# Kernel optimization log

Hardware: AMD Instinct MI355X
Metric: run time of the kernel (lower is better)

## Reference

```python
import jax, jax.numpy as jnp
import numpy as np

T = 32          # n_node_types
EXTRA = 3       # input_dim = T + 3
D = 9           # perfect binary tree depth -> N = 2**D - 1 = 511 nodes/plan
N = 2 ** D - 1
EMB = 64
HID = 64
FC = 64
OUT = 8         # N_METRICS
NS = 5          # N_SAMPLES
P = 2560        # number of plans (P // NS = 512 groups)
B = 512


def setup_inputs() -> dict:
    key = jax.random.key(0)
    ks = jax.random.split(key, 8)

    def lin(k, o, i):
        return (jax.random.normal(k, (o, i), jnp.float32) / np.sqrt(i)).astype(jnp.float32)

    x0 = jax.random.normal(ks[0], (P, N, T + EXTRA), jnp.float32)
    x = jax.random.uniform(ks[1], (B, P // NS), jnp.float32)
    return {
        "x": x,
        "x0": x0,
        "W_emb": lin(ks[2], EMB, T), "b_emb": jnp.zeros((EMB,), jnp.float32),
        "W0": lin(ks[3], HID, EMB + EXTRA), "b0": jnp.zeros((HID,), jnp.float32),
        "W1": lin(ks[4], HID, EMB + EXTRA + 2 * HID), "b1": jnp.zeros((HID,), jnp.float32),
        "Wfc1": lin(ks[5], FC, HID), "bfc1": jnp.zeros((FC,), jnp.float32),
        "Wfc2": lin(ks[6], OUT, FC), "bfc2": jnp.zeros((OUT,), jnp.float32),
    }


def reference(x, x0, W_emb, b_emb, W0, b0, W1, b1, Wfc1, bfc1, Wfc2, bfc2):
    # --- enc_dnn: per-node embed + concat(extra, children hiddens) + Linear + ReLU ---
    # node_emb = emb(xi[:T]); node_input = [node_emb, xi[T:], h_children...]
    emb = jnp.einsum('pnt,et->pne', x0[..., :T], W_emb) + b_emb    # [P,N,EMB]
    feats = jnp.concatenate([emb, x0[..., T:]], axis=-1)           # [P,N,EMB+3]
    # heap layout: node i's children are 2i+1, 2i+2; level l occupies [2^l-1, 2^{l+1}-1)
    lo = 2 ** (D - 1) - 1
    h = jax.nn.relu(jnp.einsum('pnf,hf->pnh', feats[:, lo:], W0) + b0)  # leaves
    for l in range(D - 2, -1, -1):  # structural loop over tree levels (fixed, small)
        lo, n = 2 ** l - 1, 2 ** l
        f = feats[:, lo:lo + n]
        inp = jnp.concatenate([f, h[:, 0::2], h[:, 1::2]], axis=-1)  # [emb|extra|h_left|h_right]
        h = jax.nn.relu(jnp.einsum('pnf,hf->pnh', inp, W1) + b1)
    h0 = h[:, 0]                                                   # root hidden, [P,HID]
    # --- agg_weight ---
    mean_h = h0.reshape(-1, NS, HID).mean(axis=1)                  # [P/NS, HID]
    weighted = x @ mean_h                                          # [B, HID]
    hid = jax.nn.relu(weighted @ Wfc1.T + bfc1)
    return hid @ Wfc2.T + bfc2                                     # [B, OUT]
```

## Files before the change

### kernel.cpp

```cpp
#include <hip/hip_runtime.h>
#include <hip/hip_bf16.h>


typedef __attribute__((ext_vector_type(8))) short s8v;
typedef __attribute__((ext_vector_type(4))) float f4v;
typedef unsigned short u16;
typedef unsigned int   u32;

__device__ __forceinline__ u16 f2bf(float f) {
    return __builtin_bit_cast(u16, __float2bfloat16(f));
}
__device__ __forceinline__ f4v mfma16(s8v a, s8v b, f4v c) {
    return __builtin_amdgcn_mfma_f32_16x16x32_bf16(a, b, c, 0, 0, 0);
}
#define SWZ(r) ((((r) & 1) | (((r) >> 1) & 6)) << 3)

__device__ __forceinline__ u32 pk2(float a, float b) {
    return (u32)f2bf(fmaxf(a, 0.f)) | ((u32)f2bf(fmaxf(b, 0.f)) << 16);
}
__device__ __forceinline__ s8v pkfrag(f4v h0, f4v h1) {
    int4 d;
    d.x = (int)pk2(h0[0], h0[1]); d.y = (int)pk2(h0[2], h0[3]);
    d.z = (int)pk2(h1[0], h1[1]); d.w = (int)pk2(h1[2], h1[3]);
    return __builtin_bit_cast(s8v, d);
}
__device__ __forceinline__ s8v xB0(const float* __restrict__ xr, int lq) {
    float4 A = *(const float4*)(xr + lq * 8);
    float4 B = *(const float4*)(xr + lq * 8 + 4);
    s8v r;
    r[0]=(short)f2bf(A.x); r[1]=(short)f2bf(A.y); r[2]=(short)f2bf(A.z); r[3]=(short)f2bf(A.w);
    r[4]=(short)f2bf(B.x); r[5]=(short)f2bf(B.y); r[6]=(short)f2bf(B.z); r[7]=(short)f2bf(B.w);
    return r;
}
__device__ __forceinline__ s8v xB1(const float* __restrict__ xr, int lq) {
    s8v r = (s8v){0,0,0,0,0,0,0,0};
    if (lq == 0) {
        float4 T = *(const float4*)(xr + 31);
        r[0]=(short)f2bf(T.y); r[1]=(short)f2bf(T.z); r[2]=(short)f2bf(T.w);
    }
    return r;
}
__device__ __forceinline__ s8v wread(const u16* w, int stride, int row, int ks, int lq) {
    return *(const s8v*)(w + row * stride + ks * 32 + lq * 8);
}
__device__ __forceinline__ f4v bias4(const float* __restrict__ b) {
    float4 t = *(const float4*)b; return (f4v){t.x, t.y, t.z, t.w};
}
__device__ __forceinline__ int sigp(int rho, int s, int h) {
    return 32*s + 4*h + ((rho & 12) << 1) + (rho & 3);
}

__global__ void prep_kernel(const float* __restrict__ W_emb, const float* __restrict__ b_emb,
                            const float* __restrict__ W0, const float* __restrict__ b0,
                            const float* __restrict__ W1, const float* __restrict__ b1,
                            u16* __restrict__ wt1, u16* __restrict__ wt0,
                            float* __restrict__ b1p, float* __restrict__ b0p)
{
    int idx = blockIdx.x * 256 + threadIdx.x;
    if (idx < 64 * 192) {
        int h = idx / 192, k = idx % 192;
        float v;
        if (k < 32) { v = 0.f; for (int e = 0; e < 64; e++) v = fmaf(W1[h*195+e], W_emb[e*32+k], v); }
        else if (k < 35)  v = W1[h*195 + 64 + (k - 32)];
        else if (k < 64)  v = 0.f;
        else              v = W1[h*195 + 67 + (k - 64)];
        wt1[h*192 + k] = f2bf(v);
    } else if (idx < 64*192 + 64*64) {
        int j = idx - 64*192; int h = j >> 6, k = j & 63;
        float v;
        if (k < 32)      { v = 0.f; for (int e = 0; e < 64; e++) v = fmaf(W0[h*67+e], W_emb[e*32+k], v); }
        else if (k < 35)   v = W0[h*67 + 64 + (k - 32)];
        else               v = 0.f;
        wt0[h*64 + k] = f2bf(v);
    } else if (idx < 64*192 + 64*64 + 64) {
        int h = idx - (64*192 + 64*64);
        float v = b1[h];
        for (int e = 0; e < 64; e++) v = fmaf(W1[h*195+e], b_emb[e], v);
        b1p[h] = v;
    } else if (idx < 64*192 + 64*64 + 128) {
        int h = idx - (64*192 + 64*64 + 64);
        float v = b0[h];
        for (int e = 0; e < 64; e++) v = fmaf(W0[h*67+e], b_emb[e], v);
        b0p[h] = v;
    }
}

__global__ __launch_bounds__(512, 2) void tree_chain(
    const float* __restrict__ x0,
    const u16* __restrict__ wt1g, const u16* __restrict__ wt0g,
    const float* __restrict__ b1p, const float* __restrict__ b0p,
    u16* __restrict__ h4)
{
    __shared__ __align__(16) u16 wt1s[64 * 200];
    __shared__ __align__(16) u16 wt0s[64 * 40 + 64];
    __shared__ __align__(16) u16 buf6[2 * 64 * 64];

    const int tid = threadIdx.x;
    const int l   = tid & 63;
    const int w   = tid >> 6;
    const int lq  = l >> 4;
    const int rho = l & 15;
    const int tsel = w >> 2;
    const int c    = w & 3;
    const int tree = blockIdx.x * 2 + tsel;
    const float* xb = x0 + (size_t)tree * 511 * 35;

    {
        u32* d1 = (u32*)wt1s; const u32* s1 = (const u32*)wt1g;
        #pragma unroll
        for (int t = 0; t < 12; t++) {
            int i = t*512 + tid;
            int row = i / 96, kk = i - row*96;
            d1[row*100 + kk] = s1[row*96 + kk];
        }
        u32* d0 = (u32*)wt0s; const u32* s0 = (const u32*)wt0g;
        #pragma unroll
        for (int t = 0; t < 3; t++) {
            int i = t*512 + tid;
            if (i < 1280) { int row = i / 20, kk = i - row*20; d0[row*20 + kk] = s0[row*32 + kk]; }
        }
        if (tid < 32) ((u32*)(wt0s + 64*40))[tid] = 0;
    }
    __syncthreads();

    s8v TLf[4][2];
    {
        s8v WL[4][2]; f4v bL[4];
        #pragma unroll
        for (int i = 0; i < 4; i++) {
            int s = i >> 1, h = i & 1;
            int sg = sigp(rho, s, h);
            WL[i][0] = wread(wt0s, 40, sg, 0, lq);
            WL[i][1] = wread(wt0s, 40, sg, 1, lq);
            bL[i] = bias4(b0p + 32*s + 8*lq + 4*h);
        }
        #pragma unroll
        for (int q = 0; q < 4; q++) {
            const float* xr = xb + (size_t)(255 + 64*c + 4*rho + q) * 35;
            s8v xa = xB0(xr, lq), xt = xB1(xr, lq);
            f4v a0 = bL[0], a1 = bL[1], a2 = bL[2], a3 = bL[3];
            a0 = mfma16(WL[0][0], xa, a0); a0 = mfma16(WL[0][1], xt, a0);
            a1 = mfma16(WL[1][0], xa, a1); a1 = mfma16(WL[1][1], xt, a1);
            a2 = mfma16(WL[2][0], xa, a2); a2 = mfma16(WL[2][1], xt, a2);
            a3 = mfma16(WL[3][0], xa, a3); a3 = mfma16(WL[3][1], xt, a3);
            TLf[q][0] = pkfrag(a0, a1);
            TLf[q][1] = pkfrag(a2, a3);
        }
    }

    s8v T7E0, T7E1, T7O0, T7O1;
    {
        f4v aE[4], aO[4];
        #pragma unroll
        for (int i = 0; i < 4; i++) {
            f4v b = bias4(b1p + 32*(i>>1) + 8*lq + 4*(i&1));
            aE[i] = b; aO[i] = b;
        }
        {
            const float* xrE = xb + (size_t)(127 + 32*c + 2*rho) * 35;
            const float* xrO = xrE + 35;
            s8v xE0 = xB0(xrE, lq), xE1 = xB1(xrE, lq);
            s8v xO0 = xB0(xrO, lq), xO1 = xB1(xrO, lq);
            #pragma unroll
            for (int i = 0; i < 4; i++) {
                int sg = sigp(rho, i>>1, i&1);
                s8v w0 = wread(wt1s, 200, sg, 0, lq);
                s8v w1 = wread(wt1s, 200, sg, 1, lq);
                aE[i] = mfma16(w0, xE0, aE[i]); aE[i] = mfma16(w1, xE1, aE[i]);
                aO[i] = mfma16(w0, xO0, aO[i]); aO[i] = mfma16(w1, xO1, aO[i]);
            }
        }
        #pragma unroll
        for (int i = 0; i < 4; i++) {
            int sg = sigp(rho, i>>1, i&1);
            s8v w2 = wread(wt1s, 200, sg, 2, lq);
            s8v w3 = wread(wt1s, 200, sg, 3, lq);
            s8v w4 = wread(wt1s, 200, sg, 4, lq);
            s8v w5 = wread(wt1s, 200, sg, 5, lq);
            aE[i] = mfma16(w2, TLf[0][0], aE[i]); aE[i] = mfma16(w3, TLf[0][1], aE[i]);
            aE[i] = mfma16(w4, TLf[1][0], aE[i]); aE[i] = mfma16(w5, TLf[1][1], aE[i]);
            aO[i] = mfma16(w2, TLf[2][0], aO[i]); aO[i] = mfma16(w3, TLf[2][1], aO[i]);
            aO[i] = mfma16(w4, TLf[3][0], aO[i]); aO[i] = mfma16(w5, TLf[3][1], aO[i]);
        }
        T7E0 = pkfrag(aE[0], aE[1]); T7E1 = pkfrag(aE[2], aE[3]);
        T7O0 = pkfrag(aO[0], aO[1]); T7O1 = pkfrag(aO[2], aO[3]);
    }

    {
        const float* xr6 = xb + (size_t)(63 + 16*c + rho) * 35;
        s8v x60 = xB0(xr6, lq), x61 = xB1(xr6, lq);
        u16* b6 = buf6 + tsel * 4096;
        int r6 = 16*c + rho;
        #pragma unroll
        for (int cc = 0; cc < 4; cc++) {
            f4v a = bias4(b1p + 16*cc + 4*lq);
            int sg = 16*cc + rho;
            s8v w0 = wread(wt1s, 200, sg, 0, lq);
            s8v w1 = wread(wt1s, 200, sg, 1, lq);
            s8v w2 = wread(wt1s, 200, sg, 2, lq);
            s8v w3 = wread(wt1s, 200, sg, 3, lq);
            s8v w4 = wread(wt1s, 200, sg, 4, lq);
            s8v w5 = wread(wt1s, 200, sg, 5, lq);
            a = mfma16(w0, x60, a);  a = mfma16(w1, x61, a);
            a = mfma16(w2, T7E0, a); a = mfma16(w3, T7E1, a);
            a = mfma16(w4, T7O0, a); a = mfma16(w5, T7O1, a);
            uint2 d; d.x = pk2(a[0], a[1]); d.y = pk2(a[2], a[3]);
            int col = (16*cc + 4*lq) ^ SWZ(r6);
            *(uint2*)(b6 + (size_t)r6 * 64 + col) = d;
        }
    }
    __syncthreads();

    if (c == 0) {
        const u16* b6r = buf6 + tsel * 4096;
        s8v ch5[2][2][2];
        #pragma unroll
        for (int d5 = 0; d5 < 2; d5++)
        #pragma unroll
        for (int pr = 0; pr < 2; pr++) {
            int row = 4*rho + 2*d5 + pr;
            int sw = SWZ(row);
            ch5[d5][pr][0] = *(const s8v*)(b6r + (size_t)row*64 + ((     8*lq) ^ sw));
            ch5[d5][pr][1] = *(const s8v*)(b6r + (size_t)row*64 + ((32 + 8*lq) ^ sw));
        }
        const float* xr5E = xb + (size_t)(31 + 2*rho) * 35;
        const float* xr5O = xr5E + 35;
        s8v x5E0 = xB0(xr5E, lq), x5E1 = xB1(xr5E, lq);
        s8v x5O0 = xB0(xr5O, lq), x5O1 = xB1(xr5O, lq);
        f4v aE[4], aO[4];
        #pragma unroll
        for (int i = 0; i < 4; i++) {
            f4v b = bias4(b1p + 32*(i>>1) + 8*lq + 4*(i&1));
            aE[i] = b; aO[i] = b;
        }
        #pragma unroll
        for (int i = 0; i < 4; i++) {
            int sg = sigp(rho, i>>1, i&1);
            s8v w0 = wread(wt1s, 200, sg, 0, lq);
            s8v w1 = wread(wt1s, 200, sg, 1, lq);
            s8v w2 = wread(wt1s, 200, sg, 2, lq);
            s8v w3 = wread(wt1s, 200, sg, 3, lq);
            s8v w4 = wread(wt1s, 200, sg, 4, lq);
            s8v w5 = wread(wt1s, 200, sg, 5, lq);
            aE[i] = mfma16(w0, x5E0, aE[i]); aE[i] = mfma16(w1, x5E1, aE[i]);
            aE[i] = mfma16(w2, ch5[0][0][0], aE[i]); aE[i] = mfma16(w3, ch5[0][0][1], aE[i]);
            aE[i] = mfma16(w4, ch5[0][1][0], aE[i]); aE[i] = mfma16(w5, ch5[0][1][1], aE[i]);
            aO[i] = mfma16(w0, x5O0, aO[i]); aO[i] = mfma16(w1, x5O1, aO[i]);
            aO[i] = mfma16(w2, ch5[1][0][0], aO[i]); aO[i] = mfma16(w3, ch5[1][0][1], aO[i]);
            aO[i] = mfma16(w4, ch5[1][1][0], aO[i]); aO[i] = mfma16(w5, ch5[1][1][1], aO[i]);
        }
        s8v L5E0 = pkfrag(aE[0], aE[1]), L5E1 = pkfrag(aE[2], aE[3]);
        s8v L5O0 = pkfrag(aO[0], aO[1]), L5O1 = pkfrag(aO[2], aO[3]);

        const float* xr4 = xb + (size_t)(15 + rho) * 35;
        s8v x40 = xB0(xr4, lq), x41 = xB1(xr4, lq);
        #pragma unroll
        for (int cc = 0; cc < 4; cc++) {
            f4v a = bias4(b1p + 16*cc + 4*lq);
            int sg = 16*cc + rho;
            s8v w0 = wread(wt1s, 200, sg, 0, lq);
            s8v w1 = wread(wt1s, 200, sg, 1, lq);
            s8v w2 = wread(wt1s, 200, sg, 2, lq);
            s8v w3 = wread(wt1s, 200, sg, 3, lq);
            s8v w4 = wread(wt1s, 200, sg, 4, lq);
            s8v w5 = wread(wt1s, 200, sg, 5, lq);
            a = mfma16(w0, x40, a);  a = mfma16(w1, x41, a);
            a = mfma16(w2, L5E0, a); a = mfma16(w3, L5E1, a);
            a = mfma16(w4, L5O0, a); a = mfma16(w5, L5O1, a);
            size_t base = ((size_t)tree*16 + rho) * 64 + 16*cc + 4*lq;
            *(u32*)(h4 + base)     = pk2(a[0], a[1]);
            *(u32*)(h4 + base + 2) = pk2(a[2], a[3]);
        }
    }
}

struct XL { float4 A, B, T; };
__device__ __forceinline__ s8v mk0(const XL& v) {
    s8v r;
    r[0]=(short)f2bf(v.A.x); r[1]=(short)f2bf(v.A.y); r[2]=(short)f2bf(v.A.z); r[3]=(short)f2bf(v.A.w);
    r[4]=(short)f2bf(v.B.x); r[5]=(short)f2bf(v.B.y); r[6]=(short)f2bf(v.B.z); r[7]=(short)f2bf(v.B.w);
    return r;
}
__device__ __forceinline__ s8v mk1(const XL& v) {
    s8v r = {0,0,0,0,0,0,0,0};
    r[0]=(short)f2bf(v.T.y); r[1]=(short)f2bf(v.T.z); r[2]=(short)f2bf(v.T.w);
    return r;
}

__global__ __launch_bounds__(64) void k3_tail(
    const float* __restrict__ x0,
    const u16* __restrict__ wt1, const float* __restrict__ b1p,
    const u16* __restrict__ h4, float* __restrict__ h0)
{
    __shared__ __align__(16) u16 tb0[32 * 64];
    __shared__ __align__(16) u16 tb1[32 * 64];
    const int l  = threadIdx.x;
    const int lq = l >> 4, lm = l & 15;
    const int p  = blockIdx.x;
    const float* xb = x0 + (size_t)p * 511 * 35;

    auto xload = [&](int lo) -> XL {
        const float* xr = xb + (size_t)(lo + lm) * 35;
        XL v;
        v.A = *(const float4*)(xr + lq * 8);
        v.B = *(const float4*)(xr + lq * 8 + 4);
        if (lq == 0) v.T = *(const float4*)(xr + 31);
        else         v.T = float4{0.f, 0.f, 0.f, 0.f};
        return v;
    };

    XL X3 = xload(7), X2 = xload(3), X1 = xload(1), X0v = xload(0);
    s8v ch[4];
    #pragma unroll
    for (int ks = 0; ks < 4; ks++) {
        int k0 = ks*32 + lq*8;
        int rr = 2*lm + (k0 >> 6);
        ch[ks] = *(const s8v*)(h4 + ((size_t)p*16 + rr)*64 + (k0 & 63));
    }

    s8v wB[6][4]; f4v bi[4];
    #pragma unroll
    for (int ct = 0; ct < 4; ct++) {
        int col = ct*16 + lm;
        #pragma unroll
        for (int ks = 0; ks < 6; ks++) wB[ks][ct] = *(const s8v*)(wt1 + col*192 + ks*32 + lq*8);
        float bv = b1p[col];
        bi[ct] = (f4v){bv, bv, bv, bv};
    }

    f4v acc[4];
    auto store_lds = [&](u16* buf) {
        #pragma unroll
        for (int r = 0; r < 4; r++) {
            int ro = lq*4 + r; int sw = SWZ(ro);
            #pragma unroll
            for (int ct = 0; ct < 4; ct++)
                buf[ro*64 + ((ct*16 + lm) ^ sw)] = f2bf(fmaxf(acc[ct][r], 0.f));
        }
        asm volatile("s_waitcnt lgkmcnt(0)" ::: "memory");
    };

    {
        s8v a0 = mk0(X3), a1 = mk1(X3);
        #pragma unroll
        for (int ct = 0; ct < 4; ct++) {
            acc[ct] = bi[ct];
            acc[ct] = mfma16(a0, wB[0][ct], acc[ct]);
            acc[ct] = mfma16(a1, wB[1][ct], acc[ct]);
        }
        #pragma unroll
        for (int ks = 0; ks < 4; ks++)
            #pragma unroll
            for (int ct = 0; ct < 4; ct++) acc[ct] = mfma16(ch[ks], wB[2 + ks][ct], acc[ct]);
        store_lds(tb0);
    }

    auto level = [&](const XL& xv, const u16* bufR) {
        s8v a0 = mk0(xv), a1 = mk1(xv);
        #pragma unroll
        for (int ct = 0; ct < 4; ct++) {
            acc[ct] = bi[ct];
            acc[ct] = mfma16(a0, wB[0][ct], acc[ct]);
            acc[ct] = mfma16(a1, wB[1][ct], acc[ct]);
        }
        #pragma unroll
        for (int ks = 0; ks < 4; ks++) {
            int k0 = ks*32 + lq*8;
            int rr = 2*lm + (k0 >> 6);
            s8v a = *(const s8v*)(bufR + rr*64 + ((k0 & 63) ^ SWZ(rr)));
            #pragma unroll
            for (int ct = 0; ct < 4; ct++) acc[ct] = mfma16(a, wB[2 + ks][ct], acc[ct]);
        }
    };
    level(X2, tb0); store_lds(tb1);
    level(X1, tb1); store_lds(tb0);
    level(X0v, tb0);
    if (lq == 0) {
        #pragma unroll
        for (int ct = 0; ct < 4; ct++)
            h0[(size_t)p*64 + ct*16 + lm] = fmaxf(acc[ct][0], 0.f);
    }
}

__global__ void mean_kernel(const float* __restrict__ h0, float* __restrict__ mh)
{
    int idx = blockIdx.x * blockDim.x + threadIdx.x;
    if (idx < 512 * 64) {
        int g = idx >> 6, h = idx & 63;
        float s = 0.f;
        #pragma unroll
        for (int q = 0; q < 5; q++) s += h0[(size_t)(g * 5 + q) * 64 + h];
        mh[idx] = s * 0.2f;
    }
}

__global__ __launch_bounds__(64) void head_kernel(const float* __restrict__ x,
                                                  const float* __restrict__ mh,
                                                  const float* __restrict__ Wfc1,
                                                  const float* __restrict__ bfc1,
                                                  const float* __restrict__ Wfc2,
                                                  const float* __restrict__ bfc2,
                                                  float* __restrict__ out)
{
    __shared__ float sw[64];
    __shared__ float sh[64];
    int b = blockIdx.x, h = threadIdx.x;

    float a0 = 0.f, a1 = 0.f, a2 = 0.f, a3 = 0.f;
    const float* xr = x + (size_t)b * 512;
    for (int g = 0; g < 512; g += 4) {
        a0 = fmaf(xr[g + 0], mh[(g + 0) * 64 + h], a0);
        a1 = fmaf(xr[g + 1], mh[(g + 1) * 64 + h], a1);
        a2 = fmaf(xr[g + 2], mh[(g + 2) * 64 + h], a2);
        a3 = fmaf(xr[g + 3], mh[(g + 3) * 64 + h], a3);
    }
    sw[h] = (a0 + a1) + (a2 + a3);
    __syncthreads();

    float acc = bfc1[h];
    #pragma unroll 8
    for (int k = 0; k < 64; k++) acc = fmaf(Wfc1[h * 64 + k], sw[k], acc);
    sh[h] = fmaxf(acc, 0.f);
    __syncthreads();

    if (h < 8) {
        float o = bfc2[h];
        #pragma unroll 8
        for (int f = 0; f < 64; f++) o = fmaf(Wfc2[h * 64 + f], sh[f], o);
        out[(size_t)b * 8 + h] = o;
    }
}

extern "C" void kernel_launch(void* const* d_in, const int* in_sizes, int n_in,
                              void* d_out, int out_size, void* d_ws, size_t ws_size,
                              hipStream_t stream)
{
    (void)in_sizes; (void)n_in; (void)out_size; (void)ws_size;
    const float* x     = (const float*)d_in[0];
    const float* x0    = (const float*)d_in[1];
    const float* W_emb = (const float*)d_in[2];
    const float* b_emb = (const float*)d_in[3];
    const float* W0    = (const float*)d_in[4];
    const float* b0    = (const float*)d_in[5];
    const float* W1    = (const float*)d_in[6];
    const float* b1    = (const float*)d_in[7];
    const float* Wfc1  = (const float*)d_in[8];
    const float* bfc1  = (const float*)d_in[9];
    const float* Wfc2  = (const float*)d_in[10];
    const float* bfc2  = (const float*)d_in[11];
    float* out = (float*)d_out;

    u16* wt1   = (u16*)d_ws;
    u16* wt0   = wt1 + 64 * 192;
    float* b1p = (float*)(wt0 + 64 * 64);
    float* b0p = b1p + 64;
    u16* h4    = (u16*)(b0p + 64);
    float* h0  = (float*)(h4 + (size_t)2560 * 16 * 64);
    float* mh  = h0 + 2560 * 64;

    prep_kernel<<<65, 256, 0, stream>>>(W_emb, b_emb, W0, b0, W1, b1, wt1, wt0, b1p, b0p);
    tree_chain<<<1280, 512, 0, stream>>>(x0, wt1, wt0, b1p, b0p, h4);
    k3_tail<<<2560, 64, 0, stream>>>(x0, wt1, b1p, h4, h0);
    mean_kernel<<<128, 256, 0, stream>>>(h0, mh);
    head_kernel<<<512, 64, 0, stream>>>(x, mh, Wfc1, bfc1, Wfc2, bfc2, out);
}
```

Before: 95.69 us.

## Fuse tree tail into chain kernel and process four trees per block

Merges the separate tail kernel (levels 3..0) into the main tree kernel, so the level-4 hiddens stay in LDS instead of round-tripping through a global h4 buffer, and one launch is removed. Each block now handles four trees, with each wave pair processing two trees through the leaf-to-level-6 stages. The weight load into LDS is amortised over twice as many trees. Levels 5 and below now run on only 4 of 8 waves, one tree per wave, which leaves half the block idle in the tail. LDS use also grows, which may lower occupancy.

Measured after the change: 88.57 us, median of 2. 7.4% less time.

```diff
diff --git a/kernel.cpp b/kernel.cpp
--- a/kernel.cpp
+++ b/kernel.cpp
@@ -85,25 +85,27 @@
     }
 }
 
-__global__ __launch_bounds__(512, 2) void tree_chain(
+__global__ __launch_bounds__(512, 2) void tree_all(
     const float* __restrict__ x0,
     const u16* __restrict__ wt1g, const u16* __restrict__ wt0g,
     const float* __restrict__ b1p, const float* __restrict__ b0p,
-    u16* __restrict__ h4)
+    float* __restrict__ h0out)
 {
     __shared__ __align__(16) u16 wt1s[64 * 200];
     __shared__ __align__(16) u16 wt0s[64 * 40 + 64];
-    __shared__ __align__(16) u16 buf6[2 * 64 * 64];
+    __shared__ __align__(16) u16 buf6[4 * 64 * 64];
 
     const int tid = threadIdx.x;
     const int l   = tid & 63;
     const int w   = tid >> 6;
     const int lq  = l >> 4;
     const int rho = l & 15;
-    const int tsel = w >> 2;
+    const int pair = w >> 2;
     const int c    = w & 3;
-    const int tree = blockIdx.x * 2 + tsel;
-    const float* xb = x0 + (size_t)tree * 511 * 35;
+    const int tA = blockIdx.x * 4 + 2 * pair;
+    const int tB = tA + 1;
+    const float* xbA = x0 + (size_t)tA * 511 * 35;
+    const float* xbB = x0 + (size_t)tB * 511 * 35;
 
     {
         u32* d1 = (u32*)wt1s; const u32* s1 = (const u32*)wt1g;
@@ -123,77 +125,96 @@
     }
     __syncthreads();
 
-    s8v TLf[4][2];
+    s8v TLA[4][2], TLB[4][2];
     {
         s8v WL[4][2]; f4v bL[4];
         #pragma unroll
         for (int i = 0; i < 4; i++) {
-            int s = i >> 1, h = i & 1;
-            int sg = sigp(rho, s, h);
+            int sg = sigp(rho, i >> 1, i & 1);
             WL[i][0] = wread(wt0s, 40, sg, 0, lq);
             WL[i][1] = wread(wt0s, 40, sg, 1, lq);
-            bL[i] = bias4(b0p + 32*s + 8*lq + 4*h);
+            bL[i] = bias4(b0p + 32*(i>>1) + 8*lq + 4*(i&1));
         }
         #pragma unroll
         for (int q = 0; q < 4; q++) {
-            const float* xr = xb + (size_t)(255 + 64*c + 4*rho + q) * 35;
-            s8v xa = xB0(xr, lq), xt = xB1(xr, lq);
-            f4v a0 = bL[0], a1 = bL[1], a2 = bL[2], a3 = bL[3];
-            a0 = mfma16(WL[0][0], xa, a0); a0 = mfma16(WL[0][1], xt, a0);
-            a1 = mfma16(WL[1][0], xa, a1); a1 = mfma16(WL[1][1], xt, a1);
-            a2 = mfma16(WL[2][0], xa, a2); a2 = mfma16(WL[2][1], xt, a2);
-            a3 = mfma16(WL[3][0], xa, a3); a3 = mfma16(WL[3][1], xt, a3);
-            TLf[q][0] = pkfrag(a0, a1);
-            TLf[q][1] = pkfrag(a2, a3);
-        }
-    }
-
-    s8v T7E0, T7E1, T7O0, T7O1;
+            const float* xrA = xbA + (size_t)(255 + 64*c + 4*rho + q) * 35;
+            const float* xrB = xbB + (size_t)(255 + 64*c + 4*rho + q) * 35;
+            s8v xaA = xB0(xrA, lq), xtA = xB1(xrA, lq);
+            s8v xaB = xB0(xrB, lq), xtB = xB1(xrB, lq);
+            f4v aA[4], aB[4];
+            #pragma unroll
+            for (int i = 0; i < 4; i++) { aA[i] = bL[i]; aB[i] = bL[i]; }
+            #pragma unroll
+            for (int i = 0; i < 4; i++) {
+                aA[i] = mfma16(WL[i][0], xaA, aA[i]);
+                aA[i] = mfma16(WL[i][1], xtA, aA[i]);
+                aB[i] = mfma16(WL[i][0], xaB, aB[i]);
+                aB[i] = mfma16(WL[i][1], xtB, aB[i]);
+            }
+            TLA[q][0] = pkfrag(aA[0], aA[1]); TLA[q][1] = pkfrag(aA[2], aA[3]);
+            TLB[q][0] = pkfrag(aB[0], aB[1]); TLB[q][1] = pkfrag(aB[2], aB[3]);
+        }
+    }
+
+    s8v A7[4], B7[4];
     {
-        f4v aE[4], aO[4];
+        f4v aAE[4], aAO[4], aBE[4], aBO[4];
         #pragma unroll
         for (int i = 0; i < 4; i++) {
             f4v b = bias4(b1p + 32*(i>>1) + 8*lq + 4*(i&1));
-            aE[i] = b; aO[i] = b;
+            aAE[i] = b; aAO[i] = b; aBE[i] = b; aBO[i] = b;
         }
         {
-            const float* xrE = xb + (size_t)(127 + 32*c + 2*rho) * 35;
-            const float* xrO = xrE + 35;
-            s8v xE0 = xB0(xrE, lq), xE1 = xB1(xrE, lq);
-            s8v xO0 = xB0(xrO, lq), xO1 = xB1(xrO, lq);
+            const float* xrAE = xbA + (size_t)(127 + 32*c + 2*rho) * 35;
+            const float* xrBE = xbB + (size_t)(127 + 32*c + 2*rho) * 35;
+            s8v xAE0 = xB0(xrAE, lq),      xAE1 = xB1(xrAE, lq);
+            s8v xAO0 = xB0(xrAE + 35, lq), xAO1 = xB1(xrAE + 35, lq);
+            s8v xBE0 = xB0(xrBE, lq),      xBE1 = xB1(xrBE, lq);
+            s8v xBO0 = xB0(xrBE + 35, lq), xBO1 = xB1(xrBE + 35, lq);
             #pragma unroll
             for (int i = 0; i < 4; i++) {
-                int sg = sigp(rho, i>>1, i&1);
+                int sg = sigp(rho, i >> 1, i & 1);
                 s8v w0 = wread(wt1s, 200, sg, 0, lq);
                 s8v w1 = wread(wt1s, 200, sg, 1, lq);
-                aE[i] = mfma16(w0, xE0, aE[i]); aE[i] = mfma16(w1, xE1, aE[i]);
-                aO[i] = mfma16(w0, xO0, aO[i]); aO[i] = mfma16(w1, xO1, aO[i]);
+                aAE[i] = mfma16(w0, xAE0, aAE[i]); aAE[i] = mfma16(w1, xAE1, aAE[i]);
+                aAO[i] = mfma16(w0, xAO0, aAO[i]); aAO[i] = mfma16(w1, xAO1, aAO[i]);
+                aBE[i] = mfma16(w0, xBE0, aBE[i]); aBE[i] = mfma16(w1, xBE1, aBE[i]);
+                aBO[i] = mfma16(w0, xBO0, aBO[i]); aBO[i] = mfma16(w1, xBO1, aBO[i]);
             }
         }
         #pragma unroll
         for (int i = 0; i < 4; i++) {
-            int sg = sigp(rho, i>>1, i&1);
+            int sg = sigp(rho, i >> 1, i & 1);
             s8v w2 = wread(wt1s, 200, sg, 2, lq);
             s8v w3 = wread(wt1s, 200, sg, 3, lq);
             s8v w4 = wread(wt1s, 200, sg, 4, lq);
             s8v w5 = wread(wt1s, 200, sg, 5, lq);
-            aE[i] = mfma16(w2, TLf[0][0], aE[i]); aE[i] = mfma16(w3, TLf[0][1], aE[i]);
-            aE[i] = mfma16(w4, TLf[1][0], aE[i]); aE[i] = mfma16(w5, TLf[1][1], aE[i]);
-            aO[i] = mfma16(w2, TLf[2][0], aO[i]); aO[i] = mfma16(w3, TLf[2][1], aO[i]);
-            aO[i] = mfma16(w4, TLf[3][0], aO[i]); aO[i] = mfma16(w5, TLf[3][1], aO[i]);
-        }
-        T7E0 = pkfrag(aE[0], aE[1]); T7E1 = pkfrag(aE[2], aE[3]);
-        T7O0 = pkfrag(aO[0], aO[1]); T7O1 = pkfrag(aO[2], aO[3]);
+            aAE[i] = mfma16(w2, TLA[0][0], aAE[i]); aAE[i] = mfma16(w3, TLA[0][1], aAE[i]);
+            aAE[i] = mfma16(w4, TLA[1][0], aAE[i]); aAE[i] = mfma16(w5, TLA[1][1], aAE[i]);
+            aAO[i] = mfma16(w2, TLA[2][0], aAO[i]); aAO[i] = mfma16(w3, TLA[2][1], aAO[i]);
+            aAO[i] = mfma16(w4, TLA[3][0], aAO[i]); aAO[i] = mfma16(w5, TLA[3][1], aAO[i]);
+            aBE[i] = mfma16(w2, TLB[0][0], aBE[i]); aBE[i] = mfma16(w3, TLB[0][1], aBE[i]);
+            aBE[i] = mfma16(w4, TLB[1][0], aBE[i]); aBE[i] = mfma16(w5, TLB[1][1], aBE[i]);
+            aBO[i] = mfma16(w2, TLB[2][0], aBO[i]); aBO[i] = mfma16(w3, TLB[2][1], aBO[i]);
+            aBO[i] = mfma16(w4, TLB[3][0], aBO[i]); aBO[i] = mfma16(w5, TLB[3][1], aBO[i]);
+        }
+        A7[0] = pkfrag(aAE[0], aAE[1]); A7[1] = pkfrag(aAE[2], aAE[3]);
+        A7[2] = pkfrag(aAO[0], aAO[1]); A7[3] = pkfrag(aAO[2], aAO[3]);
+        B7[0] = pkfrag(aBE[0], aBE[1]); B7[1] = pkfrag(aBE[2], aBE[3]);
+        B7[2] = pkfrag(aBO[0], aBO[1]); B7[3] = pkfrag(aBO[2], aBO[3]);
     }
 
     {
-        const float* xr6 = xb + (size_t)(63 + 16*c + rho) * 35;
-        s8v x60 = xB0(xr6, lq), x61 = xB1(xr6, lq);
-        u16* b6 = buf6 + tsel * 4096;
+        const float* xrA6 = xbA + (size_t)(63 + 16*c + rho) * 35;
+        const float* xrB6 = xbB + (size_t)(63 + 16*c + rho) * 35;
+        s8v xA0 = xB0(xrA6, lq), xA1 = xB1(xrA6, lq);
+        s8v xBv0 = xB0(xrB6, lq), xBv1 = xB1(xrB6, lq);
+        u16* slA = buf6 + (2*pair) * 4096;
+        u16* slB = slA + 4096;
         int r6 = 16*c + rho;
+        int sw6 = SWZ(r6);
         #pragma unroll
         for (int cc = 0; cc < 4; cc++) {
-            f4v a = bias4(b1p + 16*cc + 4*lq);
             int sg = 16*cc + rho;
             s8v w0 = wread(wt1s, 200, sg, 0, lq);
             s8v w1 = wread(wt1s, 200, sg, 1, lq);
@@ -201,18 +222,28 @@
             s8v w3 = wread(wt1s, 200, sg, 3, lq);
             s8v w4 = wread(wt1s, 200, sg, 4, lq);
             s8v w5 = wread(wt1s, 200, sg, 5, lq);
-            a = mfma16(w0, x60, a);  a = mfma16(w1, x61, a);
-            a = mfma16(w2, T7E0, a); a = mfma16(w3, T7E1, a);
-            a = mfma16(w4, T7O0, a); a = mfma16(w5, T7O1, a);
-            uint2 d; d.x = pk2(a[0], a[1]); d.y = pk2(a[2], a[3]);
-            int col = (16*cc + 4*lq) ^ SWZ(r6);
-            *(uint2*)(b6 + (size_t)r6 * 64 + col) = d;
+            f4v bb = bias4(b1p + 16*cc + 4*lq);
+            f4v aA = bb, aB = bb;
+            aA = mfma16(w0, xA0, aA);  aA = mfma16(w1, xA1, aA);
+            aA = mfma16(w2, A7[0], aA); aA = mfma16(w3, A7[1], aA);
+            aA = mfma16(w4, A7[2], aA); aA = mfma16(w5, A7[3], aA);
+            aB = mfma16(w0, xBv0, aB); aB = mfma16(w1, xBv1, aB);
+            aB = mfma16(w2, B7[0], aB); aB = mfma16(w3, B7[1], aB);
+            aB = mfma16(w4, B7[2], aB); aB = mfma16(w5, B7[3], aB);
+            int col = (16*cc + 4*lq) ^ sw6;
+            uint2 dA; dA.x = pk2(aA[0], aA[1]); dA.y = pk2(aA[2], aA[3]);
+            uint2 dB; dB.x = pk2(aB[0], aB[1]); dB.y = pk2(aB[2], aB[3]);
+            *(uint2*)(slA + (size_t)r6 * 64 + col) = dA;
+            *(uint2*)(slB + (size_t)r6 * 64 + col) = dB;
         }
     }
     __syncthreads();
 
-    if (c == 0) {
-        const u16* b6r = buf6 + tsel * 4096;
+    if (w < 4) {
+        const int tree = blockIdx.x * 4 + w;
+        u16* slice = buf6 + w * 4096;
+        const float* xb = x0 + (size_t)tree * 511 * 35;
+
         s8v ch5[2][2][2];
         #pragma unroll
         for (int d5 = 0; d5 < 2; d5++)
@@ -220,13 +251,12 @@
         for (int pr = 0; pr < 2; pr++) {
             int row = 4*rho + 2*d5 + pr;
             int sw = SWZ(row);
-            ch5[d5][pr][0] = *(const s8v*)(b6r + (size_t)row*64 + ((     8*lq) ^ sw));
-            ch5[d5][pr][1] = *(const s8v*)(b6r + (size_t)row*64 + ((32 + 8*lq) ^ sw));
+            ch5[d5][pr][0] = *(const s8v*)(slice + (size_t)row*64 + ((     8*lq) ^ sw));
+            ch5[d5][pr][1] = *(const s8v*)(slice + (size_t)row*64 + ((32 + 8*lq) ^ sw));
         }
         const float* xr5E = xb + (size_t)(31 + 2*rho) * 35;
-        const float* xr5O = xr5E + 35;
-        s8v x5E0 = xB0(xr5E, lq), x5E1 = xB1(xr5E, lq);
-        s8v x5O0 = xB0(xr5O, lq), x5O1 = xB1(xr5O, lq);
+        s8v x5E0 = xB0(xr5E, lq),      x5E1 = xB1(xr5E, lq);
+        s8v x5O0 = xB0(xr5E + 35, lq), x5O1 = xB1(xr5E + 35, lq);
         f4v aE[4], aO[4];
         #pragma unroll
         for (int i = 0; i < 4; i++) {
@@ -235,7 +265,7 @@
         }
         #pragma unroll
         for (int i = 0; i < 4; i++) {
-            int sg = sigp(rho, i>>1, i&1);
+            int sg = sigp(rho, i >> 1, i & 1);
             s8v w0 = wread(wt1s, 200, sg, 0, lq);
             s8v w1 = wread(wt1s, 200, sg, 1, lq);
             s8v w2 = wread(wt1s, 200, sg, 2, lq);
@@ -252,133 +282,77 @@
         s8v L5E0 = pkfrag(aE[0], aE[1]), L5E1 = pkfrag(aE[2], aE[3]);
         s8v L5O0 = pkfrag(aO[0], aO[1]), L5O1 = pkfrag(aO[2], aO[3]);
 
-        const float* xr4 = xb + (size_t)(15 + rho) * 35;
-        s8v x40 = xB0(xr4, lq), x41 = xB1(xr4, lq);
-        #pragma unroll
-        for (int cc = 0; cc < 4; cc++) {
-            f4v a = bias4(b1p + 16*cc + 4*lq);
-            int sg = 16*cc + rho;
-            s8v w0 = wread(wt1s, 200, sg, 0, lq);
-            s8v w1 = wread(wt1s, 200, sg, 1, lq);
-            s8v w2 = wread(wt1s, 200, sg, 2, lq);
-            s8v w3 = wread(wt1s, 200, sg, 3, lq);
-            s8v w4 = wread(wt1s, 200, sg, 4, lq);
-            s8v w5 = wread(wt1s, 200, sg, 5, lq);
-            a = mfma16(w0, x40, a);  a = mfma16(w1, x41, a);
-            a = mfma16(w2, L5E0, a); a = mfma16(w3, L5E1, a);
-            a = mfma16(w4, L5O0, a); a = mfma16(w5, L5O1, a);
-            size_t base = ((size_t)tree*16 + rho) * 64 + 16*cc + 4*lq;
-            *(u32*)(h4 + base)     = pk2(a[0], a[1]);
-            *(u32*)(h4 + base + 2) = pk2(a[2], a[3]);
-        }
-    }
-}
-
-struct XL { float4 A, B, T; };
-__device__ __forceinline__ s8v mk0(const XL& v) {
-    s8v r;
-    r[0]=(short)f2bf(v.A.x); r[1]=(short)f2bf(v.A.y); r[2]=(short)f2bf(v.A.z); r[3]=(short)f2bf(v.A.w);
-    r[4]=(short)f2bf(v.B.x); r[5]=(short)f2bf(v.B.y); r[6]=(short)f2bf(v.B.z); r[7]=(short)f2bf(v.B.w);
-    return r;
-}
-__device__ __forceinline__ s8v mk1(const XL& v) {
-    s8v r = {0,0,0,0,0,0,0,0};
-    r[0]=(short)f2bf(v.T.y); r[1]=(short)f2bf(v.T.z); r[2]=(short)f2bf(v.T.w);
-    return r;
-}
-
-__global__ __launch_bounds__(64) void k3_tail(
-    const float* __restrict__ x0,
-    const u16* __restrict__ wt1, const float* __restrict__ b1p,
-    const u16* __restrict__ h4, float* __restrict__ h0)
-{
-    __shared__ __align__(16) u16 tb0[32 * 64];
-    __shared__ __align__(16) u16 tb1[32 * 64];
-    const int l  = threadIdx.x;
-    const int lq = l >> 4, lm = l & 15;
-    const int p  = blockIdx.x;
-    const float* xb = x0 + (size_t)p * 511 * 35;
-
-    auto xload = [&](int lo) -> XL {
-        const float* xr = xb + (size_t)(lo + lm) * 35;
-        XL v;
-        v.A = *(const float4*)(xr + lq * 8);
-        v.B = *(const float4*)(xr + lq * 8 + 4);
-        if (lq == 0) v.T = *(const float4*)(xr + 31);
-        else         v.T = float4{0.f, 0.f, 0.f, 0.f};
-        return v;
-    };
-
-    XL X3 = xload(7), X2 = xload(3), X1 = xload(1), X0v = xload(0);
-    s8v ch[4];
-    #pragma unroll
-    for (int ks = 0; ks < 4; ks++) {
-        int k0 = ks*32 + lq*8;
-        int rr = 2*lm + (k0 >> 6);
-        ch[ks] = *(const s8v*)(h4 + ((size_t)p*16 + rr)*64 + (k0 & 63));
-    }
-
-    s8v wB[6][4]; f4v bi[4];
-    #pragma unroll
-    for (int ct = 0; ct < 4; ct++) {
-        int col = ct*16 + lm;
-        #pragma unroll
-        for (int ks = 0; ks < 6; ks++) wB[ks][ct] = *(const s8v*)(wt1 + col*192 + ks*32 + lq*8);
-        float bv = b1p[col];
-        bi[ct] = (f4v){bv, bv, bv, bv};
-    }
-
-    f4v acc[4];
-    auto store_lds = [&](u16* buf) {
-        #pragma unroll
-        for (int r = 0; r < 4; r++) {
-            int ro = lq*4 + r; int sw = SWZ(ro);
+        {
+            const float* xr4 = xb + (size_t)(15 + rho) * 35;
+            s8v x40 = xB0(xr4, lq), x41 = xB1(xr4, lq);
+            int sw4 = SWZ(rho);
+            #pragma unroll
+            for (int cc = 0; cc < 4; cc++) {
+                int sg = 16*cc + rho;
+                s8v w0 = wread(wt1s, 200, sg, 0, lq);
+                s8v w1 = wread(wt1s, 200, sg, 1, lq);
+                s8v w2 = wread(wt1s, 200, sg, 2, lq);
+                s8v w3 = wread(wt1s, 200, sg, 3, lq);
+                s8v w4 = wread(wt1s, 200, sg, 4, lq);
+                s8v w5 = wread(wt1s, 200, sg, 5, lq);
+                f4v a = bias4(b1p + 16*cc + 4*lq);
+                a = mfma16(w0, x40, a);  a = mfma16(w1, x41, a);
+                a = mfma16(w2, L5E0, a); a = mfma16(w3, L5E1, a);
+                a = mfma16(w4, L5O0, a); a = mfma16(w5, L5O1, a);
+                int col = (16*cc + 4*lq) ^ sw4;
+                uint2 d; d.x = pk2(a[0], a[1]); d.y = pk2(a[2], a[3]);
+                *(uint2*)(slice + (size_t)rho * 64 + col) = d;
+            }
+        }
+        asm volatile("s_waitcnt lgkmcnt(0)" ::: "memory");
+
+        u16* tb0 = slice + 32 * 64;
+        u16* tb1 = slice;
+        float bv[4];
+        #pragma unroll
+        for (int ct = 0; ct < 4; ct++) bv[ct] = b1p[ct*16 + rho];
+        f4v acc[4];
+
+        auto tlevel = [&](int lo, const u16* cb) {
+            const float* xr = xb + (size_t)(lo + rho) * 35;
+            s8v a0 = xB0(xr, lq), a1 = xB1(xr, lq);
+            #pragma unroll
+            for (int ct = 0; ct < 4; ct++) acc[ct] = (f4v){bv[ct], bv[ct], bv[ct], bv[ct]};
+            #pragma unroll
+            for (int ct = 0; ct < 4; ct++) {
+                acc[ct] = mfma16(a0, wread(wt1s, 200, ct*16 + rho, 0, lq), acc[ct]);
+                acc[ct] = mfma16(a1, wread(wt1s, 200, ct*16 + rho, 1, lq), acc[ct]);
+            }
+            #pragma unroll
+            for (int ks = 0; ks < 4; ks++) {
+                int k0 = ks*32 + lq*8;
+                int rr = 2*rho + (k0 >> 6);
+                s8v ach = *(const s8v*)(cb + (size_t)rr*64 + ((k0 & 63) ^ SWZ(rr)));
+                #pragma unroll
+                for (int ct = 0; ct < 4; ct++)
+                    acc[ct] = mfma16(ach, wread(wt1s, 200, ct*16 + rho, 2 + ks, lq), acc[ct]);
+            }
+        };
+        auto tstore = [&](u16* buf) {
+            #pragma unroll
+            for (int r = 0; r < 4; r++) {
+                int ro = lq*4 + r; int sw = SWZ(ro);
+                #pragma unroll
+                for (int ct = 0; ct < 4; ct++)
+                    buf[ro*64 + ((ct*16 + rho) ^ sw)] = f2bf(fmaxf(acc[ct][r], 0.f));
+            }
+            asm volatile("s_waitcnt lgkmcnt(0)" ::: "memory");
+        };
+
+        tlevel(7, slice);  tstore(tb0);
+        tlevel(3, tb0);    tstore(tb1);
+        tlevel(1, tb1);    tstore(tb0);
+        tlevel(0, tb0);
+        if (lq == 0) {
             #pragma unroll
             for (int ct = 0; ct < 4; ct++)
-                buf[ro*64 + ((ct*16 + lm) ^ sw)] = f2bf(fmaxf(acc[ct][r], 0.f));
-        }
-        asm volatile("s_waitcnt lgkmcnt(0)" ::: "memory");
-    };
-
-    {
-        s8v a0 = mk0(X3), a1 = mk1(X3);
-        #pragma unroll
-        for (int ct = 0; ct < 4; ct++) {
-            acc[ct] = bi[ct];
-            acc[ct] = mfma16(a0, wB[0][ct], acc[ct]);
-            acc[ct] = mfma16(a1, wB[1][ct], acc[ct]);
-        }
-        #pragma unroll
-        for (int ks = 0; ks < 4; ks++)
-            #pragma unroll
-            for (int ct = 0; ct < 4; ct++) acc[ct] = mfma16(ch[ks], wB[2 + ks][ct], acc[ct]);
-        store_lds(tb0);
-    }
-
-    auto level = [&](const XL& xv, const u16* bufR) {
-        s8v a0 = mk0(xv), a1 = mk1(xv);
-        #pragma unroll
-        for (int ct = 0; ct < 4; ct++) {
-            acc[ct] = bi[ct];
-            acc[ct] = mfma16(a0, wB[0][ct], acc[ct]);
-            acc[ct] = mfma16(a1, wB[1][ct], acc[ct]);
-        }
-        #pragma unroll
-        for (int ks = 0; ks < 4; ks++) {
-            int k0 = ks*32 + lq*8;
-            int rr = 2*lm + (k0 >> 6);
-            s8v a = *(const s8v*)(bufR + rr*64 + ((k0 & 63) ^ SWZ(rr)));
-            #pragma unroll
-            for (int ct = 0; ct < 4; ct++) acc[ct] = mfma16(a, wB[2 + ks][ct], acc[ct]);
-        }
-    };
-    level(X2, tb0); store_lds(tb1);
-    level(X1, tb1); store_lds(tb0);
-    level(X0v, tb0);
-    if (lq == 0) {
-        #pragma unroll
-        for (int ct = 0; ct < 4; ct++)
-            h0[(size_t)p*64 + ct*16 + lm] = fmaxf(acc[ct][0], 0.f);
+                h0out[(size_t)tree*64 + ct*16 + rho] = fmaxf(acc[ct][0], 0.f);
+        }
     }
 }
 
@@ -454,13 +428,11 @@
     u16* wt0   = wt1 + 64 * 192;
     float* b1p = (float*)(wt0 + 64 * 64);
     float* b0p = b1p + 64;
-    u16* h4    = (u16*)(b0p + 64);
-    float* h0  = (float*)(h4 + (size_t)2560 * 16 * 64);
+    float* h0  = b0p + 64;
     float* mh  = h0 + 2560 * 64;
 
     prep_kernel<<<65, 256, 0, stream>>>(W_emb, b_emb, W0, b0, W1, b1, wt1, wt0, b1p, b0p);
-    tree_chain<<<1280, 512, 0, stream>>>(x0, wt1, wt0, b1p, b0p, h4);
-    k3_tail<<<2560, 64, 0, stream>>>(x0, wt1, b1p, h4, h0);
+    tree_all<<<640, 512, 0, stream>>>(x0, wt1, wt0, b1p, b0p, h0);
     mean_kernel<<<128, 256, 0, stream>>>(h0, mh);
     head_kernel<<<512, 64, 0, stream>>>(x, mh, Wfc1, bfc1, Wfc2, bfc2, out);
 }
```
